# Kernel optimization log

Hardware: AMD Instinct MI355X
Metric: run time of the kernel (lower is better)

The kernel has to match this reference:

```python
import jax, jax.numpy as jnp
import numpy as np

NUM_TOKENS_SCORE = 64
NUM_HEADS = 16
NUM_KV_HEADS = 4
HEAD_SIZE = 128
SCALE = 0.08838834764831845  # 1/sqrt(128)


def setup_inputs() -> dict:
    key = jax.random.key(0)
    k1, k2, k3 = jax.random.split(key, 3)
    B, S = 2, 2048
    total = B * S
    return {
        "query": jax.random.normal(k1, (total, NUM_HEADS * HEAD_SIZE), dtype=jnp.float32),
        "key": jax.random.normal(k2, (total, NUM_KV_HEADS * HEAD_SIZE), dtype=jnp.float32),
        "value": jax.random.normal(k3, (total, NUM_KV_HEADS * HEAD_SIZE), dtype=jnp.float32),
        "batch_size": B,
        "seq_len": S,
    }


def reference(query, key, value, batch_size, seq_len):
    """Prompt-phase SparsePagedAttention: varlen causal GQA attention (equal
    prompt lengths -> dense [B,S] layout) plus the fused softmax score-sum over
    the last NUM_TOKENS_SCORE query rows used for KV-cache pruning."""
    B, S = batch_size, seq_len
    H, Hk, D = NUM_HEADS, NUM_KV_HEADS, HEAD_SIZE
    rep = H // Hk  # queries per kv head (head_mapping via repeat_interleave)

    q = query.reshape(B, S, H, D)
    k = jnp.repeat(key.reshape(B, S, Hk, D), rep, axis=2)    # [B,S,H,D]
    v = jnp.repeat(value.reshape(B, S, Hk, D), rep, axis=2)  # [B,S,H,D]

    scores = jnp.einsum('bqhd,bkhd->bhqk', q, k) * SCALE      # [B,H,S,S]
    causal = jnp.tril(jnp.ones((S, S), dtype=bool))
    scores = jnp.where(causal[None, None], scores, jnp.finfo(scores.dtype).min)
    probs = jax.nn.softmax(scores, axis=-1)                   # [B,H,S,S]

    out = jnp.einsum('bhqk,bkhd->bqhd', probs, v).reshape(B * S, H * D)
    # triton_fused_softmax_sum: sum softmax probs over last NUM_TOKENS_SCORE queries
    score_sum = probs[:, :, S - NUM_TOKENS_SCORE:, :].sum(axis=2)  # [B,H,S]
    return out, score_sum
```

## Files before the change

### kernel.cpp

```cpp
#include <hip/hip_runtime.h>


#define BB 2
#define SS 2048
#define NH 16
#define NKV 4
#define DD 128
#define TILE_SH 4096

typedef __attribute__((ext_vector_type(8))) short bf16x8;
typedef __attribute__((ext_vector_type(4))) float f32x4;

constexpr float SCL = 0.08838834764831845f * 1.4426950408889634f;

__device__ __forceinline__ short f2bf(float f) {
  union { float f; unsigned u; } v; v.f = f;
  unsigned r = v.u + 0x7FFFu + ((v.u >> 16) & 1u);
  return (short)(r >> 16);
}

__device__ __forceinline__ unsigned pack2bf(float a, float b) {
  union { float f; unsigned u; } x, y; x.f = a; y.f = b;
  return __builtin_amdgcn_perm(y.u, x.u, 0x07060302);
}

__device__ __forceinline__ void gl_lds16(const void* g, void* l) {
  __builtin_amdgcn_global_load_lds(
      (const __attribute__((address_space(1))) unsigned*)g,
      (__attribute__((address_space(3))) unsigned*)l, 16, 0, 0);
}

__global__ void prep(const float* __restrict__ K, const float* __restrict__ V,
                     short* __restrict__ Kb, short* __restrict__ Vb) {
  const int p = blockIdx.x;
  const int b = p >> 8, hk = (p >> 6) & 3, kt = p & 63;
  const int tid = threadIdx.x;
  const int k0 = kt * 32;
  short* kb = Kb + ((size_t)((b * 4 + hk) * 64 + kt)) * TILE_SH;
  short* vb = Vb + ((size_t)((b * 4 + hk) * 64 + kt)) * TILE_SH;
  {
    const int k = tid & 31, chb = tid >> 5;
    const float* src = K + ((size_t)(b * SS + k0 + k) * NKV + hk) * DD;
#pragma unroll
    for (int i = 0; i < 2; ++i) {
      const int ch = chb + i * 8;
      const float* s = src + ch * 8;
      float4 f0 = *(const float4*)s;
      float4 f1 = *(const float4*)(s + 4);
      bf16x8 t;
      t[0] = f2bf(f0.x); t[1] = f2bf(f0.y); t[2] = f2bf(f0.z); t[3] = f2bf(f0.w);
      t[4] = f2bf(f1.x); t[5] = f2bf(f1.y); t[6] = f2bf(f1.z); t[7] = f2bf(f1.w);
      *(bf16x8*)(kb + (ch * 32 + k) * 8) = t;
    }
  }
  {
    const int d = tid & 127, kcb = tid >> 7;
#pragma unroll
    for (int i = 0; i < 2; ++i) {
      const int kc = kcb + i * 2;
      const float* s = V + ((size_t)(b * SS + k0 + kc * 8) * NKV + hk) * DD + d;
      bf16x8 t;
#pragma unroll
      for (int e = 0; e < 8; ++e) t[e] = f2bf(s[(size_t)e * (NKV * DD)]);
      *(bf16x8*)(vb + (kc * 128 + d) * 8) = t;
    }
  }
}

__global__ __launch_bounds__(256, 4) void fa2(
    const float* __restrict__ Q, const short* __restrict__ Kb,
    const short* __restrict__ Vb, float* __restrict__ Out,
    float* __restrict__ wsl) {
  __shared__ bf16x8 kv[2][1024];
  __shared__ short ldsP[4][640];

  const int tid = threadIdx.x;
  const int w = tid >> 6, lane = tid & 63;
  const int c = lane & 15, qd = lane >> 4;

  const int i = blockIdx.x;
  const int g = i >> 8, cc = i & 255;
  const int bh = cc >> 3, jp = cc & 7;
  const int qt = (g == 0) ? jp : (g == 1) ? 31 - jp : (g == 2) ? 8 + jp : 23 - jp;
  const int b = bh >> 4, h = bh & 15, hk = h >> 2;

  const char* KT = (const char*)(Kb + ((size_t)(b * 4 + hk)) * 64 * TILE_SH);
  const char* VT = (const char*)(Vb + ((size_t)(b * 4 + hk)) * 64 * TILE_SH);

  auto stage = [&](int kt, int bi) {
    const char* sk = KT + (size_t)kt * 8192 + w * 2048 + lane * 16;
    const char* sv = VT + (size_t)kt * 8192 + w * 2048 + lane * 16;
    char* dk = (char*)kv[bi] + w * 2048;
    char* dv = dk + 8192;
#pragma unroll
    for (int t = 0; t < 2; ++t) {
      gl_lds16(sk + t * 1024, dk + t * 1024);
      gl_lds16(sv + t * 1024, dv + t * 1024);
    }
  };

  stage(0, 0);

  const int nk = 2 * qt + 2;

  const float* qrow = Q + ((size_t)(b * SS + qt * 64 + w * 16 + c) * NH + h) * DD;
  bf16x8 qf[4];
#pragma unroll
  for (int ks = 0; ks < 4; ++ks) {
    const float* p = qrow + ks * 32 + qd * 8;
    float4 f0 = *(const float4*)p;
    float4 f1 = *(const float4*)(p + 4);
    bf16x8 t;
    t[0] = f2bf(f0.x * SCL); t[1] = f2bf(f0.y * SCL);
    t[2] = f2bf(f0.z * SCL); t[3] = f2bf(f0.w * SCL);
    t[4] = f2bf(f1.x * SCL); t[5] = f2bf(f1.y * SCL);
    t[6] = f2bf(f1.z * SCL); t[7] = f2bf(f1.w * SCL);
    qf[ks] = t;
  }

  f32x4 o[8];
#pragma unroll
  for (int dt = 0; dt < 8; ++dt) { o[dt][0] = 0.f; o[dt][1] = 0.f; o[dt][2] = 0.f; o[dt][3] = 0.f; }
  float l_part = 0.f;

  for (int kt = 0; kt < nk; ++kt) {
    __syncthreads();
    const int cb = kt & 1;
    if (kt + 1 < nk) stage(kt + 1, cb ^ 1);

    const bf16x8* bK = kv[cb];
    const bf16x8* bV = kv[cb] + 512;

    f32x4 st0 = {0.f, 0.f, 0.f, 0.f}, st1 = {0.f, 0.f, 0.f, 0.f};
#pragma unroll
    for (int ks = 0; ks < 4; ++ks) {
      const int chz = (ks * 4 + qd) * 32;
      bf16x8 a0 = bK[chz + c];
      bf16x8 a1 = bK[chz + 16 + c];
      st0 = __builtin_amdgcn_mfma_f32_16x16x32_bf16(a0, qf[ks], st0, 0, 0, 0);
      st1 = __builtin_amdgcn_mfma_f32_16x16x32_bf16(a1, qf[ks], st1, 0, 0, 0);
    }

    float pr[8];
#pragma unroll
    for (int r = 0; r < 4; ++r) { pr[r] = exp2f(st0[r]); pr[4 + r] = exp2f(st1[r]); }
    const int koff = kt * 32 - qt * 64;
    if (koff >= 0) {
      const int qrl = w * 16 + c;
#pragma unroll
      for (int mt = 0; mt < 2; ++mt)
#pragma unroll
        for (int r = 0; r < 4; ++r)
          if (koff + mt * 16 + qd * 4 + r > qrl) pr[mt * 4 + r] = 0.f;
    }
#pragma unroll
    for (int x = 0; x < 8; ++x) l_part += pr[x];

    short* pp = ldsP[w] + c * 40;
#pragma unroll
    for (int mt = 0; mt < 2; ++mt) {
      union { short4 s4; unsigned u[2]; } pk;
      pk.u[0] = pack2bf(pr[mt * 4 + 0], pr[mt * 4 + 1]);
      pk.u[1] = pack2bf(pr[mt * 4 + 2], pr[mt * 4 + 3]);
      *(short4*)(pp + mt * 16 + qd * 4) = pk.s4;
    }
    __asm__ volatile("s_waitcnt lgkmcnt(0)" ::: "memory");
    bf16x8 pf = *(const bf16x8*)(pp + qd * 8);

#pragma unroll
    for (int dt = 0; dt < 8; ++dt)
      o[dt] = __builtin_amdgcn_mfma_f32_16x16x32_bf16(bV[qd * 128 + dt * 16 + c],
                                                      pf, o[dt], 0, 0, 0);
  }

  float l = l_part;
  l += __shfl_xor(l, 16);
  l += __shfl_xor(l, 32);
  const float linv = 1.f / l;

  float* orow = Out + ((size_t)(b * SS + qt * 64 + w * 16 + c) * NH + h) * DD;
#pragma unroll
  for (int dt = 0; dt < 8; ++dt) {
    float4 ov;
    ov.x = o[dt][0] * linv; ov.y = o[dt][1] * linv;
    ov.z = o[dt][2] * linv; ov.w = o[dt][3] * linv;
    *(float4*)(orow + dt * 16 + qd * 4) = ov;
  }
  if (qt == 31 && qd == 0)
    wsl[bh * 64 + w * 16 + c] = l;
}

__global__ __launch_bounds__(256, 2) void score(
    const float* __restrict__ Q, const short* __restrict__ Kb,
    const float* __restrict__ wsl, float* __restrict__ out2) {
  __shared__ float ldsS[4][64];
  const int tid = threadIdx.x;
  const int w = tid >> 6, lane = tid & 63;
  const int c = lane & 15, qd = lane >> 4;
  const int bh = blockIdx.x & 31, kt = blockIdx.x >> 5;
  const int b = bh >> 4, h = bh & 15, hk = h >> 2;
  const int q0 = SS - 64;

  const float* qrow = Q + ((size_t)(b * SS + q0 + w * 16 + c) * NH + h) * DD;
  bf16x8 qf[4];
#pragma unroll
  for (int ks = 0; ks < 4; ++ks) {
    const float* p = qrow + ks * 32 + qd * 8;
    float4 f0 = *(const float4*)p;
    float4 f1 = *(const float4*)(p + 4);
    bf16x8 t;
    t[0] = f2bf(f0.x * SCL); t[1] = f2bf(f0.y * SCL);
    t[2] = f2bf(f0.z * SCL); t[3] = f2bf(f0.w * SCL);
    t[4] = f2bf(f1.x * SCL); t[5] = f2bf(f1.y * SCL);
    t[6] = f2bf(f1.z * SCL); t[7] = f2bf(f1.w * SCL);
    qf[ks] = t;
  }
  float linv[4];
  const int r0 = bh * 64 + w * 16 + qd * 4;
#pragma unroll
  for (int r = 0; r < 4; ++r) linv[r] = 1.f / wsl[r0 + r];

  const bf16x8* kb = (const bf16x8*)Kb + ((size_t)(b * 4 + hk) * 64 + kt * 2) * 512;
  f32x4 s[4];
#pragma unroll
  for (int nt = 0; nt < 4; ++nt) { s[nt][0] = 0.f; s[nt][1] = 0.f; s[nt][2] = 0.f; s[nt][3] = 0.f; }
#pragma unroll
  for (int ks = 0; ks < 4; ++ks) {
#pragma unroll
    for (int nt = 0; nt < 4; ++nt) {
      bf16x8 kf = kb[(nt >> 1) * 512 + (ks * 4 + qd) * 32 + (nt & 1) * 16 + c];
      s[nt] = __builtin_amdgcn_mfma_f32_16x16x32_bf16(qf[ks], kf, s[nt], 0, 0, 0);
    }
  }
  const bool diag = (kt == 31);
  float cs[4] = {0.f, 0.f, 0.f, 0.f};
#pragma unroll
  for (int nt = 0; nt < 4; ++nt) {
#pragma unroll
    for (int r = 0; r < 4; ++r) {
      float pv = exp2f(s[nt][r]) * linv[r];
      if (diag && nt * 16 + c > w * 16 + qd * 4 + r) pv = 0.f;
      cs[nt] += pv;
    }
    cs[nt] += __shfl_xor(cs[nt], 16);
    cs[nt] += __shfl_xor(cs[nt], 32);
  }
  if (lane < 16) {
#pragma unroll
    for (int nt = 0; nt < 4; ++nt) ldsS[w][nt * 16 + c] = cs[nt];
  }
  __syncthreads();
  if (tid < 64)
    out2[(size_t)bh * SS + kt * 64 + tid] =
        ldsS[0][tid] + ldsS[1][tid] + ldsS[2][tid] + ldsS[3][tid];
}

extern "C" void kernel_launch(void* const* d_in, const int* in_sizes, int n_in,
                              void* d_out, int out_size, void* d_ws, size_t ws_size,
                              hipStream_t stream) {
  const float* Q = (const float*)d_in[0];
  const float* K = (const float*)d_in[1];
  const float* V = (const float*)d_in[2];
  float* out = (float*)d_out;
  float* out2 = out + (size_t)BB * SS * NH * DD;

  short* Kb = (short*)d_ws;
  const size_t tsz = (size_t)2 * 4 * 64 * TILE_SH;
  short* Vb = Kb + tsz;
  float* wsl = (float*)(Vb + tsz);

  hipLaunchKernelGGL(prep, dim3(512), dim3(256), 0, stream, K, V, Kb, Vb);
  hipLaunchKernelGGL(fa2, dim3(1024), dim3(256), 0, stream, Q, Kb, Vb, out, wsl);
  hipLaunchKernelGGL(score, dim3(1024), dim3(256), 0, stream, Q, Kb, wsl, out2);
}
```

Baseline: 160.6 us.

## Split long causal query tiles across two KV halves and combine partials

Result: slower. 173.8 us (+8.2%).

```diff
diff --git a/kernel.cpp b/kernel.cpp
--- a/kernel.cpp
+++ b/kernel.cpp
@@ -67,10 +67,16 @@
   }
 }
 
+__constant__ unsigned char RK2SLOT[48] = {
+    15, 46, 47, 44, 45, 14, 42, 43, 40, 41, 13, 38, 39, 36, 37, 12,
+    34, 35, 32, 33, 11, 30, 31, 28, 29, 10, 26, 27, 24, 25, 9,  22,
+    23, 20, 21, 8,  18, 19, 16, 17, 7,  6,  5,  4,  3,  2,  1,  0};
+
 __global__ __launch_bounds__(256, 4) void fa2(
     const float* __restrict__ Q, const short* __restrict__ Kb,
     const short* __restrict__ Vb, float* __restrict__ Out,
-    float* __restrict__ wsl) {
+    float* __restrict__ Ob, float* __restrict__ l0a, float* __restrict__ l1a,
+    float* __restrict__ wsl, const int mode) {
   __shared__ bf16x8 kv[2][1024];
   __shared__ short ldsP[4][640];
 
@@ -78,10 +84,27 @@
   const int w = tid >> 6, lane = tid & 63;
   const int c = lane & 15, qd = lane >> 4;
 
-  const int i = blockIdx.x;
-  const int g = i >> 8, cc = i & 255;
-  const int bh = cc >> 3, jp = cc & 7;
-  const int qt = (g == 0) ? jp : (g == 1) ? 31 - jp : (g == 2) ? 8 + jp : 23 - jp;
+  int qt, kb0, nit, part, bh;
+  if (mode) {
+    bh = blockIdx.x & 31;
+    const int rank = blockIdx.x >> 5;
+    const int slot = RK2SLOT[rank];
+    if (slot < 16) {
+      qt = slot; kb0 = 0; nit = 2 * qt + 2; part = 0;
+    } else {
+      const int s = slot - 16;
+      qt = 16 + (s >> 1);
+      if (s & 1) { kb0 = qt + 1; nit = qt + 1; part = 2; }
+      else       { kb0 = 0;      nit = qt + 1; part = 1; }
+    }
+  } else {
+    const int i = blockIdx.x;
+    const int g = i >> 8, cc = i & 255;
+    bh = cc >> 3;
+    const int jp = cc & 7;
+    qt = (g == 0) ? jp : (g == 1) ? 31 - jp : (g == 2) ? 8 + jp : 23 - jp;
+    kb0 = 0; nit = 2 * qt + 2; part = 0;
+  }
   const int b = bh >> 4, h = bh & 15, hk = h >> 2;
 
   const char* KT = (const char*)(Kb + ((size_t)(b * 4 + hk)) * 64 * TILE_SH);
@@ -99,9 +122,7 @@
     }
   };
 
-  stage(0, 0);
-
-  const int nk = 2 * qt + 2;
+  stage(kb0, 0);
 
   const float* qrow = Q + ((size_t)(b * SS + qt * 64 + w * 16 + c) * NH + h) * DD;
   bf16x8 qf[4];
@@ -123,10 +144,11 @@
   for (int dt = 0; dt < 8; ++dt) { o[dt][0] = 0.f; o[dt][1] = 0.f; o[dt][2] = 0.f; o[dt][3] = 0.f; }
   float l_part = 0.f;
 
-  for (int kt = 0; kt < nk; ++kt) {
+  for (int it = 0; it < nit; ++it) {
+    const int kt = kb0 + it;
     __syncthreads();
-    const int cb = kt & 1;
-    if (kt + 1 < nk) stage(kt + 1, cb ^ 1);
+    const int cb = it & 1;
+    if (it + 1 < nit) stage(kt + 1, cb ^ 1);
 
     const bf16x8* bK = kv[cb];
     const bf16x8* bV = kv[cb] + 512;
@@ -176,18 +198,53 @@
   float l = l_part;
   l += __shfl_xor(l, 16);
   l += __shfl_xor(l, 32);
-  const float linv = 1.f / l;
-
-  float* orow = Out + ((size_t)(b * SS + qt * 64 + w * 16 + c) * NH + h) * DD;
-#pragma unroll
-  for (int dt = 0; dt < 8; ++dt) {
-    float4 ov;
-    ov.x = o[dt][0] * linv; ov.y = o[dt][1] * linv;
-    ov.z = o[dt][2] * linv; ov.w = o[dt][3] * linv;
-    *(float4*)(orow + dt * 16 + qd * 4) = ov;
-  }
-  if (qt == 31 && qd == 0)
-    wsl[bh * 64 + w * 16 + c] = l;
+
+  if (part == 0) {
+    const float linv = 1.f / l;
+    float* orow = Out + ((size_t)(b * SS + qt * 64 + w * 16 + c) * NH + h) * DD;
+#pragma unroll
+    for (int dt = 0; dt < 8; ++dt) {
+      float4 ov;
+      ov.x = o[dt][0] * linv; ov.y = o[dt][1] * linv;
+      ov.z = o[dt][2] * linv; ov.w = o[dt][3] * linv;
+      *(float4*)(orow + dt * 16 + qd * 4) = ov;
+    }
+    if (!mode && qt == 31 && qd == 0)
+      wsl[bh * 64 + w * 16 + c] = l;
+  } else {
+    const int qoff = (qt - 16) * 64 + w * 16 + c;
+    float* dst = (part == 1)
+        ? Out + ((size_t)(b * SS + qt * 64 + w * 16 + c) * NH + h) * DD
+        : Ob + ((size_t)(bh * 1024 + qoff)) * DD;
+#pragma unroll
+    for (int dt = 0; dt < 8; ++dt)
+      *(f32x4*)(dst + dt * 16 + qd * 4) = o[dt];
+    if (qd == 0) {
+      float* la = (part == 1) ? l0a : l1a;
+      la[bh * 1024 + qoff] = l;
+    }
+  }
+}
+
+__global__ __launch_bounds__(256) void combine(
+    float* __restrict__ Out, const float* __restrict__ Ob,
+    const float* __restrict__ l0a, const float* __restrict__ l1a,
+    float* __restrict__ wsl) {
+  const int t = blockIdx.x * 256 + threadIdx.x;
+  const int row = t >> 5;
+  const int d4 = (t & 31) * 4;
+  const int bh = row >> 10, qp = row & 1023;
+  const int b = bh >> 4, h = bh & 15;
+  const float lsum = l0a[row] + l1a[row];
+  const float li = 1.f / lsum;
+  float* po = Out + ((size_t)(b * SS + 1024 + qp) * NH + h) * DD + d4;
+  const float4 a = *(const float4*)po;
+  const float4 cc = *(const float4*)(Ob + (size_t)row * DD + d4);
+  float4 r;
+  r.x = (a.x + cc.x) * li; r.y = (a.y + cc.y) * li;
+  r.z = (a.z + cc.z) * li; r.w = (a.w + cc.w) * li;
+  *(float4*)po = r;
+  if (qp >= 960 && (t & 31) == 0) wsl[bh * 64 + (qp - 960)] = lsum;
 }
 
 __global__ __launch_bounds__(256, 2) void score(
@@ -267,9 +324,21 @@
   short* Kb = (short*)d_ws;
   const size_t tsz = (size_t)2 * 4 * 64 * TILE_SH;
   short* Vb = Kb + tsz;
-  float* wsl = (float*)(Vb + tsz);
+  float* aux = (float*)(Vb + tsz);
+
+  float* Ob = aux;
+  float* l0 = Ob + (size_t)32 * 1024 * 128;
+  float* l1 = l0 + 32 * 1024;
+  float* wsl_split = l1 + 32 * 1024;
+  const size_t need = (size_t)((char*)(wsl_split + 32 * 64) - (char*)d_ws);
+  const int mode = (ws_size >= need) ? 1 : 0;
+  float* wsl = mode ? wsl_split : aux;
 
   hipLaunchKernelGGL(prep, dim3(512), dim3(256), 0, stream, K, V, Kb, Vb);
-  hipLaunchKernelGGL(fa2, dim3(1024), dim3(256), 0, stream, Q, Kb, Vb, out, wsl);
+  hipLaunchKernelGGL(fa2, dim3(mode ? 1536 : 1024), dim3(256), 0, stream,
+                     Q, Kb, Vb, out, Ob, l0, l1, wsl, mode);
+  if (mode)
+    hipLaunchKernelGGL(combine, dim3(4096), dim3(256), 0, stream,
+                       out, Ob, l0, l1, wsl);
   hipLaunchKernelGGL(score, dim3(1024), dim3(256), 0, stream, Q, Kb, wsl, out2);
 }
```

## Give each fa2 wave two 16-row query subtiles to reuse K/V fragments

Applied to the files above, without the earlier changes.

Result: slower. 177.7 us (+10.6%).

```diff
diff --git a/kernel.cpp b/kernel.cpp
--- a/kernel.cpp
+++ b/kernel.cpp
@@ -67,7 +67,7 @@
   }
 }
 
-__global__ __launch_bounds__(256, 4) void fa2(
+__global__ __launch_bounds__(128, 2) void fa2(
     const float* __restrict__ Q, const short* __restrict__ Kb,
     const short* __restrict__ Vb, float* __restrict__ Out,
     float* __restrict__ wsl) {
@@ -75,7 +75,7 @@
   __shared__ short ldsP[4][640];
 
   const int tid = threadIdx.x;
-  const int w = tid >> 6, lane = tid & 63;
+  const int wv = tid >> 6, lane = tid & 63;
   const int c = lane & 15, qd = lane >> 4;
 
   const int i = blockIdx.x;
@@ -88,12 +88,12 @@
   const char* VT = (const char*)(Vb + ((size_t)(b * 4 + hk)) * 64 * TILE_SH);
 
   auto stage = [&](int kt, int bi) {
-    const char* sk = KT + (size_t)kt * 8192 + w * 2048 + lane * 16;
-    const char* sv = VT + (size_t)kt * 8192 + w * 2048 + lane * 16;
-    char* dk = (char*)kv[bi] + w * 2048;
+    const char* sk = KT + (size_t)kt * 8192 + wv * 4096 + lane * 16;
+    const char* sv = VT + (size_t)kt * 8192 + wv * 4096 + lane * 16;
+    char* dk = (char*)kv[bi] + wv * 4096;
     char* dv = dk + 8192;
 #pragma unroll
-    for (int t = 0; t < 2; ++t) {
+    for (int t = 0; t < 4; ++t) {
       gl_lds16(sk + t * 1024, dk + t * 1024);
       gl_lds16(sv + t * 1024, dv + t * 1024);
     }
@@ -103,7 +103,142 @@
 
   const int nk = 2 * qt + 2;
 
-  const float* qrow = Q + ((size_t)(b * SS + qt * 64 + w * 16 + c) * NH + h) * DD;
+  bf16x8 qf[2][4];
+#pragma unroll
+  for (int qs = 0; qs < 2; ++qs) {
+    const float* qrow =
+        Q + ((size_t)(b * SS + qt * 64 + wv * 32 + qs * 16 + c) * NH + h) * DD;
+#pragma unroll
+    for (int ks = 0; ks < 4; ++ks) {
+      const float* p = qrow + ks * 32 + qd * 8;
+      float4 f0 = *(const float4*)p;
+      float4 f1 = *(const float4*)(p + 4);
+      bf16x8 t;
+      t[0] = f2bf(f0.x * SCL); t[1] = f2bf(f0.y * SCL);
+      t[2] = f2bf(f0.z * SCL); t[3] = f2bf(f0.w * SCL);
+      t[4] = f2bf(f1.x * SCL); t[5] = f2bf(f1.y * SCL);
+      t[6] = f2bf(f1.z * SCL); t[7] = f2bf(f1.w * SCL);
+      qf[qs][ks] = t;
+    }
+  }
+
+  f32x4 o[2][8];
+#pragma unroll
+  for (int qs = 0; qs < 2; ++qs)
+#pragma unroll
+    for (int dt = 0; dt < 8; ++dt) {
+      o[qs][dt][0] = 0.f; o[qs][dt][1] = 0.f;
+      o[qs][dt][2] = 0.f; o[qs][dt][3] = 0.f;
+    }
+  float lp[2] = {0.f, 0.f};
+
+  for (int kt = 0; kt < nk; ++kt) {
+    __syncthreads();
+    const int cb = kt & 1;
+    if (kt + 1 < nk) stage(kt + 1, cb ^ 1);
+
+    const bf16x8* bK = kv[cb];
+    const bf16x8* bV = kv[cb] + 512;
+
+    f32x4 st[2][2];
+#pragma unroll
+    for (int qs = 0; qs < 2; ++qs)
+#pragma unroll
+      for (int mt = 0; mt < 2; ++mt) {
+        st[qs][mt][0] = 0.f; st[qs][mt][1] = 0.f;
+        st[qs][mt][2] = 0.f; st[qs][mt][3] = 0.f;
+      }
+#pragma unroll
+    for (int ks = 0; ks < 4; ++ks) {
+      const int chz = (ks * 4 + qd) * 32;
+      bf16x8 a0 = bK[chz + c];
+      bf16x8 a1 = bK[chz + 16 + c];
+      st[0][0] = __builtin_amdgcn_mfma_f32_16x16x32_bf16(a0, qf[0][ks], st[0][0], 0, 0, 0);
+      st[0][1] = __builtin_amdgcn_mfma_f32_16x16x32_bf16(a1, qf[0][ks], st[0][1], 0, 0, 0);
+      st[1][0] = __builtin_amdgcn_mfma_f32_16x16x32_bf16(a0, qf[1][ks], st[1][0], 0, 0, 0);
+      st[1][1] = __builtin_amdgcn_mfma_f32_16x16x32_bf16(a1, qf[1][ks], st[1][1], 0, 0, 0);
+    }
+
+    float pr[2][8];
+#pragma unroll
+    for (int qs = 0; qs < 2; ++qs)
+#pragma unroll
+      for (int r = 0; r < 4; ++r) {
+        pr[qs][r] = exp2f(st[qs][0][r]);
+        pr[qs][4 + r] = exp2f(st[qs][1][r]);
+      }
+    const int koff = kt * 32 - qt * 64;
+    if (koff >= 0) {
+#pragma unroll
+      for (int qs = 0; qs < 2; ++qs) {
+        const int qrl = wv * 32 + qs * 16 + c;
+#pragma unroll
+        for (int mt = 0; mt < 2; ++mt)
+#pragma unroll
+          for (int r = 0; r < 4; ++r)
+            if (koff + mt * 16 + qd * 4 + r > qrl) pr[qs][mt * 4 + r] = 0.f;
+      }
+    }
+#pragma unroll
+    for (int qs = 0; qs < 2; ++qs)
+#pragma unroll
+      for (int x = 0; x < 8; ++x) lp[qs] += pr[qs][x];
+
+#pragma unroll
+    for (int qs = 0; qs < 2; ++qs) {
+      short* pp = ldsP[wv * 2 + qs] + c * 40;
+#pragma unroll
+      for (int mt = 0; mt < 2; ++mt) {
+        union { short4 s4; unsigned u[2]; } pk;
+        pk.u[0] = pack2bf(pr[qs][mt * 4 + 0], pr[qs][mt * 4 + 1]);
+        pk.u[1] = pack2bf(pr[qs][mt * 4 + 2], pr[qs][mt * 4 + 3]);
+        *(short4*)(pp + mt * 16 + qd * 4) = pk.s4;
+      }
+    }
+    __asm__ volatile("s_waitcnt lgkmcnt(0)" ::: "memory");
+    bf16x8 pf0 = *(const bf16x8*)(ldsP[wv * 2 + 0] + c * 40 + qd * 8);
+    bf16x8 pf1 = *(const bf16x8*)(ldsP[wv * 2 + 1] + c * 40 + qd * 8);
+
+#pragma unroll
+    for (int dt = 0; dt < 8; ++dt) {
+      bf16x8 av = bV[qd * 128 + dt * 16 + c];
+      o[0][dt] = __builtin_amdgcn_mfma_f32_16x16x32_bf16(av, pf0, o[0][dt], 0, 0, 0);
+      o[1][dt] = __builtin_amdgcn_mfma_f32_16x16x32_bf16(av, pf1, o[1][dt], 0, 0, 0);
+    }
+  }
+
+#pragma unroll
+  for (int qs = 0; qs < 2; ++qs) {
+    float l = lp[qs];
+    l += __shfl_xor(l, 16);
+    l += __shfl_xor(l, 32);
+    const float linv = 1.f / l;
+    float* orow =
+        Out + ((size_t)(b * SS + qt * 64 + wv * 32 + qs * 16 + c) * NH + h) * DD;
+#pragma unroll
+    for (int dt = 0; dt < 8; ++dt) {
+      float4 ov;
+      ov.x = o[qs][dt][0] * linv; ov.y = o[qs][dt][1] * linv;
+      ov.z = o[qs][dt][2] * linv; ov.w = o[qs][dt][3] * linv;
+      *(float4*)(orow + dt * 16 + qd * 4) = ov;
+    }
+    if (qt == 31 && qd == 0)
+      wsl[bh * 64 + wv * 32 + qs * 16 + c] = l;
+  }
+}
+
+__global__ __launch_bounds__(256, 2) void score(
+    const float* __restrict__ Q, const short* __restrict__ Kb,
+    const float* __restrict__ wsl, float* __restrict__ out2) {
+  __shared__ float ldsS[4][64];
+  const int tid = threadIdx.x;
+  const int w = tid >> 6, lane = tid & 63;
+  const int c = lane & 15, qd = lane >> 4;
+  const int bh = blockIdx.x & 31, kt = blockIdx.x >> 5;
+  const int b = bh >> 4, h = bh & 15, hk = h >> 2;
+  const int q0 = SS - 64;
+
+  const float* qrow = Q + ((size_t)(b * SS + q0 + w * 16 + c) * NH + h) * DD;
   bf16x8 qf[4];
 #pragma unroll
   for (int ks = 0; ks < 4; ++ks) {
@@ -117,104 +252,6 @@
     t[6] = f2bf(f1.z * SCL); t[7] = f2bf(f1.w * SCL);
     qf[ks] = t;
   }
-
-  f32x4 o[8];
-#pragma unroll
-  for (int dt = 0; dt < 8; ++dt) { o[dt][0] = 0.f; o[dt][1] = 0.f; o[dt][2] = 0.f; o[dt][3] = 0.f; }
-  float l_part = 0.f;
-
-  for (int kt = 0; kt < nk; ++kt) {
-    __syncthreads();
-    const int cb = kt & 1;
-    if (kt + 1 < nk) stage(kt + 1, cb ^ 1);
-
-    const bf16x8* bK = kv[cb];
-    const bf16x8* bV = kv[cb] + 512;
-
-    f32x4 st0 = {0.f, 0.f, 0.f, 0.f}, st1 = {0.f, 0.f, 0.f, 0.f};
-#pragma unroll
-    for (int ks = 0; ks < 4; ++ks) {
-      const int chz = (ks * 4 + qd) * 32;
-      bf16x8 a0 = bK[chz + c];
-      bf16x8 a1 = bK[chz + 16 + c];
-      st0 = __builtin_amdgcn_mfma_f32_16x16x32_bf16(a0, qf[ks], st0, 0, 0, 0);
-      st1 = __builtin_amdgcn_mfma_f32_16x16x32_bf16(a1, qf[ks], st1, 0, 0, 0);
-    }
-
-    float pr[8];
-#pragma unroll
-    for (int r = 0; r < 4; ++r) { pr[r] = exp2f(st0[r]); pr[4 + r] = exp2f(st1[r]); }
-    const int koff = kt * 32 - qt * 64;
-    if (koff >= 0) {
-      const int qrl = w * 16 + c;
-#pragma unroll
-      for (int mt = 0; mt < 2; ++mt)
-#pragma unroll
-        for (int r = 0; r < 4; ++r)
-          if (koff + mt * 16 + qd * 4 + r > qrl) pr[mt * 4 + r] = 0.f;
-    }
-#pragma unroll
-    for (int x = 0; x < 8; ++x) l_part += pr[x];
-
-    short* pp = ldsP[w] + c * 40;
-#pragma unroll
-    for (int mt = 0; mt < 2; ++mt) {
-      union { short4 s4; unsigned u[2]; } pk;
-      pk.u[0] = pack2bf(pr[mt * 4 + 0], pr[mt * 4 + 1]);
-      pk.u[1] = pack2bf(pr[mt * 4 + 2], pr[mt * 4 + 3]);
-      *(short4*)(pp + mt * 16 + qd * 4) = pk.s4;
-    }
-    __asm__ volatile("s_waitcnt lgkmcnt(0)" ::: "memory");
-    bf16x8 pf = *(const bf16x8*)(pp + qd * 8);
-
-#pragma unroll
-    for (int dt = 0; dt < 8; ++dt)
-      o[dt] = __builtin_amdgcn_mfma_f32_16x16x32_bf16(bV[qd * 128 + dt * 16 + c],
-                                                      pf, o[dt], 0, 0, 0);
-  }
-
-  float l = l_part;
-  l += __shfl_xor(l, 16);
-  l += __shfl_xor(l, 32);
-  const float linv = 1.f / l;
-
-  float* orow = Out + ((size_t)(b * SS + qt * 64 + w * 16 + c) * NH + h) * DD;
-#pragma unroll
-  for (int dt = 0; dt < 8; ++dt) {
-    float4 ov;
-    ov.x = o[dt][0] * linv; ov.y = o[dt][1] * linv;
-    ov.z = o[dt][2] * linv; ov.w = o[dt][3] * linv;
-    *(float4*)(orow + dt * 16 + qd * 4) = ov;
-  }
-  if (qt == 31 && qd == 0)
-    wsl[bh * 64 + w * 16 + c] = l;
-}
-
-__global__ __launch_bounds__(256, 2) void score(
-    const float* __restrict__ Q, const short* __restrict__ Kb,
-    const float* __restrict__ wsl, float* __restrict__ out2) {
-  __shared__ float ldsS[4][64];
-  const int tid = threadIdx.x;
-  const int w = tid >> 6, lane = tid & 63;
-  const int c = lane & 15, qd = lane >> 4;
-  const int bh = blockIdx.x & 31, kt = blockIdx.x >> 5;
-  const int b = bh >> 4, h = bh & 15, hk = h >> 2;
-  const int q0 = SS - 64;
-
-  const float* qrow = Q + ((size_t)(b * SS + q0 + w * 16 + c) * NH + h) * DD;
-  bf16x8 qf[4];
-#pragma unroll
-  for (int ks = 0; ks < 4; ++ks) {
-    const float* p = qrow + ks * 32 + qd * 8;
-    float4 f0 = *(const float4*)p;
-    float4 f1 = *(const float4*)(p + 4);
-    bf16x8 t;
-    t[0] = f2bf(f0.x * SCL); t[1] = f2bf(f0.y * SCL);
-    t[2] = f2bf(f0.z * SCL); t[3] = f2bf(f0.w * SCL);
-    t[4] = f2bf(f1.x * SCL); t[5] = f2bf(f1.y * SCL);
-    t[6] = f2bf(f1.z * SCL); t[7] = f2bf(f1.w * SCL);
-    qf[ks] = t;
-  }
   float linv[4];
   const int r0 = bh * 64 + w * 16 + qd * 4;
 #pragma unroll
@@ -270,6 +307,6 @@
   float* wsl = (float*)(Vb + tsz);
 
   hipLaunchKernelGGL(prep, dim3(512), dim3(256), 0, stream, K, V, Kb, Vb);
-  hipLaunchKernelGGL(fa2, dim3(1024), dim3(256), 0, stream, Q, Kb, Vb, out, wsl);
+  hipLaunchKernelGGL(fa2, dim3(1024), dim3(128), 0, stream, Q, Kb, Vb, out, wsl);
   hipLaunchKernelGGL(score, dim3(1024), dim3(256), 0, stream, Q, Kb, wsl, out2);
 }
```

## Triple-buffer K in LDS, load V directly to registers, remap blocks per XCD

Applied to the files above, without the earlier changes.

After: 167.8 us. 1.04x slower.

```diff
diff --git a/kernel.cpp b/kernel.cpp
--- a/kernel.cpp
+++ b/kernel.cpp
@@ -71,7 +71,7 @@
     const float* __restrict__ Q, const short* __restrict__ Kb,
     const short* __restrict__ Vb, float* __restrict__ Out,
     float* __restrict__ wsl) {
-  __shared__ bf16x8 kv[2][1024];
+  __shared__ bf16x8 kv[3][512];
   __shared__ short ldsP[4][640];
 
   const int tid = threadIdx.x;
@@ -79,31 +79,139 @@
   const int c = lane & 15, qd = lane >> 4;
 
   const int i = blockIdx.x;
-  const int g = i >> 8, cc = i & 255;
-  const int bh = cc >> 3, jp = cc & 7;
-  const int qt = (g == 0) ? jp : (g == 1) ? 31 - jp : (g == 2) ? 8 + jp : 23 - jp;
-  const int b = bh >> 4, h = bh & 15, hk = h >> 2;
+  const int xcd = i & 7;
+  const int y = i >> 3;
+  const int j = y >> 5, t = (y >> 2) & 7, hq = y & 3;
+  const int qt = (j == 0) ? t : (j == 1) ? 15 - t : (j == 2) ? 16 + t : 31 - t;
+  const int b = xcd >> 2, hk = xcd & 3, h = hk * 4 + hq;
+  const int bh = b * 16 + h;
 
   const char* KT = (const char*)(Kb + ((size_t)(b * 4 + hk)) * 64 * TILE_SH);
   const char* VT = (const char*)(Vb + ((size_t)(b * 4 + hk)) * 64 * TILE_SH);
 
   auto stage = [&](int kt, int bi) {
     const char* sk = KT + (size_t)kt * 8192 + w * 2048 + lane * 16;
-    const char* sv = VT + (size_t)kt * 8192 + w * 2048 + lane * 16;
     char* dk = (char*)kv[bi] + w * 2048;
-    char* dv = dk + 8192;
-#pragma unroll
-    for (int t = 0; t < 2; ++t) {
-      gl_lds16(sk + t * 1024, dk + t * 1024);
-      gl_lds16(sv + t * 1024, dv + t * 1024);
-    }
+    gl_lds16(sk, dk);
+    gl_lds16(sk + 1024, dk + 1024);
   };
 
+  const int nk = 2 * qt + 2;
+
   stage(0, 0);
 
-  const int nk = 2 * qt + 2;
-
   const float* qrow = Q + ((size_t)(b * SS + qt * 64 + w * 16 + c) * NH + h) * DD;
+  bf16x8 qf[4];
+#pragma unroll
+  for (int ks = 0; ks < 4; ++ks) {
+    const float* p = qrow + ks * 32 + qd * 8;
+    float4 f0 = *(const float4*)p;
+    float4 f1 = *(const float4*)(p + 4);
+    bf16x8 tq;
+    tq[0] = f2bf(f0.x * SCL); tq[1] = f2bf(f0.y * SCL);
+    tq[2] = f2bf(f0.z * SCL); tq[3] = f2bf(f0.w * SCL);
+    tq[4] = f2bf(f1.x * SCL); tq[5] = f2bf(f1.y * SCL);
+    tq[6] = f2bf(f1.z * SCL); tq[7] = f2bf(f1.w * SCL);
+    qf[ks] = tq;
+  }
+
+  stage(1, 1);
+
+  f32x4 o[8];
+#pragma unroll
+  for (int dt = 0; dt < 8; ++dt) { o[dt][0] = 0.f; o[dt][1] = 0.f; o[dt][2] = 0.f; o[dt][3] = 0.f; }
+  float l_part = 0.f;
+
+  int bcur = 0, bstage = 2;
+
+  for (int kt = 0; kt < nk; ++kt) {
+    __builtin_amdgcn_sched_barrier(0);
+    __asm__ volatile("s_waitcnt vmcnt(2)" ::: "memory");
+    __builtin_amdgcn_s_barrier();
+    __builtin_amdgcn_sched_barrier(0);
+
+    const bf16x8* bK = kv[bcur];
+
+    bf16x8 av[8];
+    const bf16x8* vg = (const bf16x8*)(VT + (size_t)kt * 8192) + (qd * 128 + c);
+#pragma unroll
+    for (int dt = 0; dt < 8; ++dt) av[dt] = vg[dt * 16];
+
+    if (kt + 2 < nk) stage(kt + 2, bstage);
+
+    f32x4 st0 = {0.f, 0.f, 0.f, 0.f}, st1 = {0.f, 0.f, 0.f, 0.f};
+#pragma unroll
+    for (int ks = 0; ks < 4; ++ks) {
+      const int chz = (ks * 4 + qd) * 32;
+      bf16x8 a0 = bK[chz + c];
+      bf16x8 a1 = bK[chz + 16 + c];
+      st0 = __builtin_amdgcn_mfma_f32_16x16x32_bf16(a0, qf[ks], st0, 0, 0, 0);
+      st1 = __builtin_amdgcn_mfma_f32_16x16x32_bf16(a1, qf[ks], st1, 0, 0, 0);
+    }
+
+    float pr[8];
+#pragma unroll
+    for (int r = 0; r < 4; ++r) { pr[r] = exp2f(st0[r]); pr[4 + r] = exp2f(st1[r]); }
+    const int koff = kt * 32 - qt * 64;
+    if (koff >= 0) {
+      const int qrl = w * 16 + c;
+#pragma unroll
+      for (int mt = 0; mt < 2; ++mt)
+#pragma unroll
+        for (int r = 0; r < 4; ++r)
+          if (koff + mt * 16 + qd * 4 + r > qrl) pr[mt * 4 + r] = 0.f;
+    }
+#pragma unroll
+    for (int x = 0; x < 8; ++x) l_part += pr[x];
+
+    short* pp = ldsP[w] + c * 40;
+#pragma unroll
+    for (int mt = 0; mt < 2; ++mt) {
+      union { short4 s4; unsigned u[2]; } pk;
+      pk.u[0] = pack2bf(pr[mt * 4 + 0], pr[mt * 4 + 1]);
+      pk.u[1] = pack2bf(pr[mt * 4 + 2], pr[mt * 4 + 3]);
+      *(short4*)(pp + mt * 16 + qd * 4) = pk.s4;
+    }
+    __asm__ volatile("s_waitcnt lgkmcnt(0)" ::: "memory");
+    bf16x8 pf = *(const bf16x8*)(pp + qd * 8);
+
+#pragma unroll
+    for (int dt = 0; dt < 8; ++dt)
+      o[dt] = __builtin_amdgcn_mfma_f32_16x16x32_bf16(av[dt], pf, o[dt], 0, 0, 0);
+
+    bcur = (bcur == 2) ? 0 : bcur + 1;
+    bstage = (bstage == 2) ? 0 : bstage + 1;
+  }
+
+  float l = l_part;
+  l += __shfl_xor(l, 16);
+  l += __shfl_xor(l, 32);
+  const float linv = 1.f / l;
+
+  float* orow = Out + ((size_t)(b * SS + qt * 64 + w * 16 + c) * NH + h) * DD;
+#pragma unroll
+  for (int dt = 0; dt < 8; ++dt) {
+    float4 ov;
+    ov.x = o[dt][0] * linv; ov.y = o[dt][1] * linv;
+    ov.z = o[dt][2] * linv; ov.w = o[dt][3] * linv;
+    *(float4*)(orow + dt * 16 + qd * 4) = ov;
+  }
+  if (qt == 31 && qd == 0)
+    wsl[bh * 64 + w * 16 + c] = l;
+}
+
+__global__ __launch_bounds__(256, 2) void score(
+    const float* __restrict__ Q, const short* __restrict__ Kb,
+    const float* __restrict__ wsl, float* __restrict__ out2) {
+  __shared__ float ldsS[4][64];
+  const int tid = threadIdx.x;
+  const int w = tid >> 6, lane = tid & 63;
+  const int c = lane & 15, qd = lane >> 4;
+  const int bh = blockIdx.x & 31, kt = blockIdx.x >> 5;
+  const int b = bh >> 4, h = bh & 15, hk = h >> 2;
+  const int q0 = SS - 64;
+
+  const float* qrow = Q + ((size_t)(b * SS + q0 + w * 16 + c) * NH + h) * DD;
   bf16x8 qf[4];
 #pragma unroll
   for (int ks = 0; ks < 4; ++ks) {
@@ -117,104 +225,6 @@
     t[6] = f2bf(f1.z * SCL); t[7] = f2bf(f1.w * SCL);
     qf[ks] = t;
   }
-
-  f32x4 o[8];
-#pragma unroll
-  for (int dt = 0; dt < 8; ++dt) { o[dt][0] = 0.f; o[dt][1] = 0.f; o[dt][2] = 0.f; o[dt][3] = 0.f; }
-  float l_part = 0.f;
-
-  for (int kt = 0; kt < nk; ++kt) {
-    __syncthreads();
-    const int cb = kt & 1;
-    if (kt + 1 < nk) stage(kt + 1, cb ^ 1);
-
-    const bf16x8* bK = kv[cb];
-    const bf16x8* bV = kv[cb] + 512;
-
-    f32x4 st0 = {0.f, 0.f, 0.f, 0.f}, st1 = {0.f, 0.f, 0.f, 0.f};
-#pragma unroll
-    for (int ks = 0; ks < 4; ++ks) {
-      const int chz = (ks * 4 + qd) * 32;
-      bf16x8 a0 = bK[chz + c];
-      bf16x8 a1 = bK[chz + 16 + c];
-      st0 = __builtin_amdgcn_mfma_f32_16x16x32_bf16(a0, qf[ks], st0, 0, 0, 0);
-      st1 = __builtin_amdgcn_mfma_f32_16x16x32_bf16(a1, qf[ks], st1, 0, 0, 0);
-    }
-
-    float pr[8];
-#pragma unroll
-    for (int r = 0; r < 4; ++r) { pr[r] = exp2f(st0[r]); pr[4 + r] = exp2f(st1[r]); }
-    const int koff = kt * 32 - qt * 64;
-    if (koff >= 0) {
-      const int qrl = w * 16 + c;
-#pragma unroll
-      for (int mt = 0; mt < 2; ++mt)
-#pragma unroll
-        for (int r = 0; r < 4; ++r)
-          if (koff + mt * 16 + qd * 4 + r > qrl) pr[mt * 4 + r] = 0.f;
-    }
-#pragma unroll
-    for (int x = 0; x < 8; ++x) l_part += pr[x];
-
-    short* pp = ldsP[w] + c * 40;
-#pragma unroll
-    for (int mt = 0; mt < 2; ++mt) {
-      union { short4 s4; unsigned u[2]; } pk;
-      pk.u[0] = pack2bf(pr[mt * 4 + 0], pr[mt * 4 + 1]);
-      pk.u[1] = pack2bf(pr[mt * 4 + 2], pr[mt * 4 + 3]);
-      *(short4*)(pp + mt * 16 + qd * 4) = pk.s4;
-    }
-    __asm__ volatile("s_waitcnt lgkmcnt(0)" ::: "memory");
-    bf16x8 pf = *(const bf16x8*)(pp + qd * 8);
-
-#pragma unroll
-    for (int dt = 0; dt < 8; ++dt)
-      o[dt] = __builtin_amdgcn_mfma_f32_16x16x32_bf16(bV[qd * 128 + dt * 16 + c],
-                                                      pf, o[dt], 0, 0, 0);
-  }
-
-  float l = l_part;
-  l += __shfl_xor(l, 16);
-  l += __shfl_xor(l, 32);
-  const float linv = 1.f / l;
-
-  float* orow = Out + ((size_t)(b * SS + qt * 64 + w * 16 + c) * NH + h) * DD;
-#pragma unroll
-  for (int dt = 0; dt < 8; ++dt) {
-    float4 ov;
-    ov.x = o[dt][0] * linv; ov.y = o[dt][1] * linv;
-    ov.z = o[dt][2] * linv; ov.w = o[dt][3] * linv;
-    *(float4*)(orow + dt * 16 + qd * 4) = ov;
-  }
-  if (qt == 31 && qd == 0)
-    wsl[bh * 64 + w * 16 + c] = l;
-}
-
-__global__ __launch_bounds__(256, 2) void score(
-    const float* __restrict__ Q, const short* __restrict__ Kb,
-    const float* __restrict__ wsl, float* __restrict__ out2) {
-  __shared__ float ldsS[4][64];
-  const int tid = threadIdx.x;
-  const int w = tid >> 6, lane = tid & 63;
-  const int c = lane & 15, qd = lane >> 4;
-  const int bh = blockIdx.x & 31, kt = blockIdx.x >> 5;
-  const int b = bh >> 4, h = bh & 15, hk = h >> 2;
-  const int q0 = SS - 64;
-
-  const float* qrow = Q + ((size_t)(b * SS + q0 + w * 16 + c) * NH + h) * DD;
-  bf16x8 qf[4];
-#pragma unroll
-  for (int ks = 0; ks < 4; ++ks) {
-    const float* p = qrow + ks * 32 + qd * 8;
-    float4 f0 = *(const float4*)p;
-    float4 f1 = *(const float4*)(p + 4);
-    bf16x8 t;
-    t[0] = f2bf(f0.x * SCL); t[1] = f2bf(f0.y * SCL);
-    t[2] = f2bf(f0.z * SCL); t[3] = f2bf(f0.w * SCL);
-    t[4] = f2bf(f1.x * SCL); t[5] = f2bf(f1.y * SCL);
-    t[6] = f2bf(f1.z * SCL); t[7] = f2bf(f1.w * SCL);
-    qf[ks] = t;
-  }
   float linv[4];
   const int r0 = bh * 64 + w * 16 + qd * 4;
 #pragma unroll
```
